# Performance work log

Hardware: AMD Instinct MI355X
Metric: run time of the kernel (lower is better)

The kernel has to match this reference:

```python
import jax, jax.numpy as jnp
import numpy as np


def _conv(x, w, b, stride, pad):
    y = jax.lax.conv_general_dilated(x, w, (stride, stride), [(pad, pad), (pad, pad)],
                                     dimension_numbers=('NCHW', 'OIHW', 'NCHW'))
    return y + b[None, :, None, None]


def _deconv(x, w, b, stride):
    # kernel == stride, VALID padding -> exact x`stride` upsample
    y = jax.lax.conv_transpose(x, w, (stride, stride), 'VALID',
                               dimension_numbers=('NCHW', 'OIHW', 'NCHW'))
    return y + b[None, :, None, None]


def _fuse(feat):
    # TransformerFusion: per-pixel scaled dot-product attention over cav axis, keep ego (cav 0)
    n, C, H, W = feat.shape
    t = feat.reshape(n, C, H * W).transpose(2, 0, 1)            # (HW, n, C)
    scores = jnp.einsum('pnc,pmc->pnm', t, t) / np.float32(np.sqrt(C))
    attn = jax.nn.softmax(scores, axis=-1)
    out = jnp.einsum('pnm,pmc->pnc', attn, t)                   # (HW, n, C)
    return out[:, 0, :].T.reshape(C, H, W)


def _sta(x, w1, w2):
    # CBAM-style channel attention: shared MLP on avg-pool and max-pool
    avg = x.mean(axis=(2, 3))                                   # (B, C)
    mx = x.max(axis=(2, 3))
    fc = lambda z: jax.nn.relu(z @ w1.T) @ w2.T
    return jax.nn.sigmoid(fc(avg) + fc(mx))[:, :, None, None]


def _forward(x, historical_x, time_delay, record_len,
             enh_w, enh_b, b0_w, b0_b, b1_w, b1_b, b2_w, b2_b,
             d0_w, d0_b, d1_w, d1_b, d2_w, d2_b, sta_w1, sta_w2):
    aoi = time_delay[0]                                         # (N + 2,)
    enw = jnp.tanh(enh_w * (1.0 / (aoi + 0.1)) + enh_b) + 1.0   # EnhanceWeight, batched
    # loop mapping: t=0 -> x[0]; t=1,2 -> historical[0,1]; t=3,4 -> x[1,2]
    x = x * jnp.stack([enw[0], enw[3], enw[4]])[:, None, None, None]
    historical_x = historical_x * enw[1:3][:, None, None, None]
    historical_x = jax.nn.relu(_conv(historical_x, b0_w, b0_b, 2, 1))  # backbone.blocks[0]

    ups = []
    x = jax.nn.relu(_conv(x, b0_w, b0_b, 2, 1))                 # level 0: (N,64,128,256)
    ups.append(_conv(_fuse(x[:record_len])[None], d0_w, d0_b, 1, 0))
    x = jax.nn.relu(_conv(x, b1_w, b1_b, 2, 1))                 # level 1: (N,128,64,128)
    ups.append(_deconv(_fuse(x[:record_len])[None], d1_w, d1_b, 2))
    x = jax.nn.relu(_conv(x, b2_w, b2_b, 2, 1))                 # level 2: (N,256,32,64)
    ups.append(_deconv(_fuse(x[:record_len])[None], d2_w, d2_b, 4))
    ups.append(historical_x[0:1])
    ups.append(historical_x[1:2])
    x_fuse = jnp.concatenate(ups, axis=1)                       # (1, 512, 128, 256)
    return _sta(x_fuse, sta_w1, sta_w2) * x_fuse


def setup_inputs() -> dict:
    key = jax.random.key(0)
    ks = jax.random.split(key, 16)
    w = lambda k, shape, fan_in: (jax.random.normal(k, shape, jnp.float32)
                                  * np.float32(np.sqrt(2.0 / fan_in)))
    N, C, H, W = 3, 64, 256, 512
    return {
        'x': jax.random.normal(ks[0], (N, C, H, W), jnp.float32),
        'historical_x': jax.random.normal(ks[1], (2, C, H, W), jnp.float32),
        'psm_single': jax.random.normal(ks[2], (N, 2, H // 2, W // 2), jnp.float32),
        'pairwise_t_matrix': jax.random.normal(ks[3], (1, N + 2, N + 2, 4, 4), jnp.float32),
        'time_delay': jax.random.uniform(ks[4], (1, N + 2), jnp.float32),
        'record_len': 3,
        'enh_w': jax.random.normal(ks[5], (), jnp.float32),
        'enh_b': jnp.zeros((), jnp.float32),
        'b0_w': w(ks[6], (64, 64, 3, 3), 64 * 9),  'b0_b': jnp.zeros((64,), jnp.float32),
        'b1_w': w(ks[7], (128, 64, 3, 3), 64 * 9), 'b1_b': jnp.zeros((128,), jnp.float32),
        'b2_w': w(ks[8], (256, 128, 3, 3), 128 * 9), 'b2_b': jnp.zeros((256,), jnp.float32),
        'd0_w': w(ks[9], (128, 64, 1, 1), 64),     'd0_b': jnp.zeros((128,), jnp.float32),
        'd1_w': w(ks[10], (128, 128, 2, 2), 128 * 4), 'd1_b': jnp.zeros((128,), jnp.float32),
        'd2_w': w(ks[11], (128, 256, 4, 4), 256 * 16), 'd2_b': jnp.zeros((128,), jnp.float32),
        'sta_w1': w(ks[12], (32, 512), 512),
        'sta_w2': w(ks[13], (512, 32), 32),
    }


def reference(x, historical_x, psm_single, pairwise_t_matrix, time_delay, record_len,
              enh_w, enh_b, b0_w, b0_b, b1_w, b1_b, b2_w, b2_b,
              d0_w, d0_b, d1_w, d1_b, d2_w, d2_b, sta_w1, sta_w2):
    # psm_single / pairwise_t_matrix are accepted but unused by HPHA's math path
    return _forward(x, historical_x, time_delay, record_len,
                    enh_w, enh_b, b0_w, b0_b, b1_w, b1_b, b2_w, b2_b,
                    d0_w, d0_b, d1_w, d1_b, d2_w, d2_b, sta_w1, sta_w2)
```

## Files before the change

### kernel.cpp

```cpp
#include <hip/hip_runtime.h>
#include <math.h>

#define HW0 32768

typedef __attribute__((ext_vector_type(8))) short short8v;
typedef __attribute__((ext_vector_type(4))) float f32x4;

static const size_t WS_SCALES = 0;
static const size_t WS_MEAN   = 64;
static const size_t WS_MAX    = 64 + 512;
static const size_t WS_GATE   = 64 + 1024;
static const size_t WS_L0X    = 2048;
static const size_t WS_L1     = WS_L0X + (size_t)3*64*128*256;
static const size_t WS_L2     = WS_L1  + (size_t)3*128*64*128;
static const size_t WS_F0     = WS_L2  + (size_t)3*256*32*64;
static const size_t WS_F1     = WS_F0  + (size_t)64*128*256;
static const size_t WS_F2     = WS_F1  + (size_t)128*64*128;
static const size_t WS_W0P    = WS_F2  + (size_t)256*32*64;
static const size_t WS_W1P    = WS_W0P + 18432;
static const size_t WS_W2P    = WS_W1P + 36864;
static const size_t WS_U0P    = WS_W2P + 147456;
static const size_t WS_U1P    = WS_U0P + 4096;
static const size_t WS_U2P    = WS_U1P + 32768;
static const size_t WS_STG    = WS_U2P + 262144;

__device__ inline unsigned short f2bf(float x) {
  unsigned u = __float_as_uint(x);
  unsigned r = ((u >> 16) & 1u) + 0x7FFFu;
  return (unsigned short)((u + r) >> 16);
}

__global__ void prep_k(const float* __restrict__ td, const float* __restrict__ ew,
                       const float* __restrict__ eb, float* __restrict__ scales) {
  int i = threadIdx.x;
  if (i < 5) {
    float e = tanhf(ew[0] * (1.0f / (td[i] + 0.1f)) + eb[0]) + 1.0f;
    const int slot[5] = {0, 3, 4, 1, 2};
    scales[slot[i]] = e;
  }
}

__global__ __launch_bounds__(256) void repack_k(const float* __restrict__ in,
                                                unsigned short* __restrict__ outh,
                                                int C, int H, int W) {
  __shared__ unsigned short lds[64 * 72];
  const int t = threadIdx.x;
  const int cbn = C >> 6;
  const int n  = blockIdx.z / cbn;
  const int cb = (blockIdx.z % cbn) << 6;
  const int h  = blockIdx.y;
  const int w0 = blockIdx.x << 6;
  const int wl = t & 63, cg = t >> 6;
  const float* ip = in + (((size_t)n * C + cb) * H + h) * W + w0;
#pragma unroll 4
  for (int cj = 0; cj < 16; ++cj) {
    int c = cg * 16 + cj;
    lds[wl * 72 + c] = f2bf(ip[(size_t)c * H * W + wl]);
  }
  __syncthreads();
  const int pw = t >> 2, ch = t & 3;
  unsigned short* op = outh + ((size_t)n * H * W + (size_t)h * W + w0 + pw) * C + cb;
#pragma unroll
  for (int it = 0; it < 2; ++it) {
    int c0 = (ch + it * 4) * 8;
    *(uint4*)(op + c0) = *(const uint4*)(lds + pw * 72 + c0);
  }
}

__global__ void pack_w_k(const float* __restrict__ W, unsigned short* __restrict__ wp,
                         int Cout, int Cin, int NK) {
  int t = blockIdx.x * 256 + threadIdx.x;
  if (t >= Cout * NK * 4) return;
  int co = t / (NK * 4); int rem = t - co * (NK * 4); int s = rem >> 2; int js = rem & 3;
  int cog = co >> 4; int l = js * 16 + (co & 15);
  unsigned short v[8];
#pragma unroll
  for (int j = 0; j < 8; ++j) {
    int k = s * 32 + js * 8 + j;
    int tap = k / Cin, ci = k - tap * Cin;
    int ky = tap / 3, kx = tap - ky * 3;
    v[j] = f2bf(W[(((size_t)co * Cin + ci) * 3 + ky) * 3 + kx]);
  }
  *(uint4*)(wp + ((size_t)(cog * NK + s) * 64 + l) * 8) = *(uint4*)v;
}

__global__ void pack_dw_k(const float* __restrict__ W, unsigned short* __restrict__ wp,
                          int M, int K, int NK, int mode) {
  int t = blockIdx.x * 256 + threadIdx.x;
  if (t >= M * NK * 4) return;
  int m = t / (NK * 4); int rem = t - m * (NK * 4); int s = rem >> 2; int js = rem & 3;
  int mt = m >> 4; int l = js * 16 + (m & 15);
  unsigned short v[8];
#pragma unroll
  for (int j = 0; j < 8; ++j) {
    int k = s * 32 + js * 8 + j;
    size_t idx;
    if (mode == 0) {
      idx = (size_t)m * K + k;
    } else if (mode == 1) {
      int o = m >> 2, r = (m >> 1) & 1, c = m & 1;
      idx = ((size_t)o * K + k) * 4 + (1 - r) * 2 + (1 - c);
    } else {
      int o = m >> 4, r = (m >> 2) & 3, c = m & 3;
      idx = ((size_t)o * K + k) * 16 + (3 - r) * 4 + (3 - c);
    }
    v[j] = f2bf(W[idx]);
  }
  *(uint4*)(wp + ((size_t)(mt * NK + s) * 64 + l) * 8) = *(uint4*)v;
}

template <int CIN, int COG>
__global__ __launch_bounds__(256) void conv_mfma_k(
    const unsigned short* __restrict__ inh, const unsigned short* __restrict__ wp,
    const float* __restrict__ bias, float* __restrict__ out,
    const float* __restrict__ scales, int Cout, int Hout, int Wout, int cogrp) {
  constexpr int NK = (9 * CIN) / 32;
  extern __shared__ unsigned short wlds[];
  const int tid = threadIdx.x, lane = tid & 63, wv = tid >> 6;
  const int Hin = Hout * 2, Win = Wout * 2;
  const int n   = blockIdx.z / cogrp;
  const int cg  = blockIdx.z % cogrp;
  const int co0 = cg * (COG * 16);
  const int h   = blockIdx.y;
  const int w0  = blockIdx.x * 64;

  {
    const float4* src = (const float4*)(wp + (size_t)(co0 >> 4) * NK * 64 * 8);
    float4* dst = (float4*)wlds;
    for (int i = tid; i < COG * NK * 64; i += 256) dst[i] = src[i];
  }
  __syncthreads();

  const int px = w0 + wv * 16 + (lane & 15);
  const int js = lane >> 4;
  const unsigned short* inp = inh + (size_t)n * CIN * Hin * Win;

  f32x4 acc[COG];
#pragma unroll
  for (int c = 0; c < COG; ++c) acc[c] = (f32x4){0.f, 0.f, 0.f, 0.f};

  const short8v bz = {0, 0, 0, 0, 0, 0, 0, 0};
  for (int s = 0; s < NK; ++s) {
    const int tap = (s * 32) / CIN;
    const int ci  = (s * 32) % CIN + js * 8;
    const int ky = tap / 3, kx = tap - ky * 3;
    const int iy = 2 * h + ky - 1;
    short8v b = bz;
    if (iy >= 0) {
      const int ix = 2 * px + kx - 1;
      const unsigned short* p = inp + ((size_t)iy * Win + (ix < 0 ? 0 : ix)) * CIN + ci;
      short8v v = *(const short8v*)p;
      if (ix >= 0) b = v;
    }
#pragma unroll
    for (int c = 0; c < COG; ++c) {
      short8v a = *(const short8v*)&wlds[((c * NK + s) * 64 + lane) * 8];
      acc[c] = __builtin_amdgcn_mfma_f32_16x16x32_bf16(a, b, acc[c], 0, 0, 0);
    }
  }

  const float sc = scales ? scales[n] : 1.0f;
#pragma unroll
  for (int c = 0; c < COG; ++c) {
#pragma unroll
    for (int r = 0; r < 4; ++r) {
      const int co = co0 + c * 16 + js * 4 + r;
      float v = fmaxf(acc[c][r] * sc + bias[co], 0.f);
      out[(((size_t)n * Cout + co) * Hout + h) * Wout + px] = v;
    }
  }
}

template <int C>
__global__ __launch_bounds__(256) void fuse2_k(const float* __restrict__ in,
                                               unsigned short* __restrict__ outh,
                                               int HW, float inv_sqrtC) {
  constexpr int LPP = C / 16;
  constexpr int PPW = 64 / LPP;
  const int tid = threadIdx.x;
  const int lane = tid & 63, wv = tid >> 6;
  const int g = lane / PPW;
  const int p = blockIdx.x * (4 * PPW) + wv * PPW + (lane % PPW);
  const float* b0 = in + (size_t)(g * 16) * HW + p;
  const float* b1 = b0 + (size_t)C * HW;
  const float* b2 = b1 + (size_t)C * HW;
  float va[16], vb[16], vd[16];
  float d00 = 0.f, d01 = 0.f, d02 = 0.f;
#pragma unroll
  for (int j = 0; j < 16; ++j) {
    va[j] = b0[(size_t)j * HW];
    vb[j] = b1[(size_t)j * HW];
    vd[j] = b2[(size_t)j * HW];
    d00 += va[j] * va[j]; d01 += va[j] * vb[j]; d02 += va[j] * vd[j];
  }
#pragma unroll
  for (int off = PPW; off < 64; off <<= 1) {
    d00 += __shfl_xor(d00, off);
    d01 += __shfl_xor(d01, off);
    d02 += __shfl_xor(d02, off);
  }
  float s0 = d00 * inv_sqrtC, s1 = d01 * inv_sqrtC, s2 = d02 * inv_sqrtC;
  float m = fmaxf(s0, fmaxf(s1, s2));
  float e0 = expf(s0 - m), e1 = expf(s1 - m), e2 = expf(s2 - m);
  float inv = 1.0f / (e0 + e1 + e2);
  float a0 = e0 * inv, a1 = e1 * inv, a2 = e2 * inv;
  unsigned short tmp[16];
#pragma unroll
  for (int j = 0; j < 16; ++j)
    tmp[j] = f2bf(a0 * va[j] + a1 * vb[j] + a2 * vd[j]);
  unsigned short* o0 = outh + (size_t)p * C + g * 16;
  *(uint4*)(o0)     = *(const uint4*)(tmp);
  *(uint4*)(o0 + 8) = *(const uint4*)(tmp + 8);
}

template <int K, int MT, int EPI>
__global__ __launch_bounds__(256) void up_mfma_k(
    const unsigned short* __restrict__ fh, const unsigned short* __restrict__ wp,
    const float* __restrict__ bias, float* __restrict__ out) {
  constexpr int NK = K / 32;
  extern __shared__ unsigned short wlds[];
  const int tid = threadIdx.x, lane = tid & 63, wv = tid >> 6;
  const int mt0 = blockIdx.y * MT;
  {
    const float4* src = (const float4*)(wp + (size_t)mt0 * NK * 64 * 8);
    float4* dst = (float4*)wlds;
    for (int i = tid; i < MT * NK * 64; i += 256) dst[i] = src[i];
  }
  __syncthreads();

  const int px = blockIdx.x * 64 + wv * 16 + (lane & 15);
  const int js = lane >> 4;
  const unsigned short* bp = fh + (size_t)px * K + js * 8;

  f32x4 acc[MT];
#pragma unroll
  for (int t = 0; t < MT; ++t) acc[t] = (f32x4){0.f, 0.f, 0.f, 0.f};

#pragma unroll
  for (int s = 0; s < NK; ++s) {
    short8v b = *(const short8v*)(bp + s * 32);
#pragma unroll
    for (int t = 0; t < MT; ++t) {
      short8v a = *(const short8v*)&wlds[((t * NK + s) * 64 + lane) * 8];
      acc[t] = __builtin_amdgcn_mfma_f32_16x16x32_bf16(a, b, acc[t], 0, 0, 0);
    }
  }

  if constexpr (EPI == 0) {
#pragma unroll
    for (int t = 0; t < MT; ++t) {
      const int o = (mt0 + t) * 16 + js * 4;
#pragma unroll
      for (int r = 0; r < 4; ++r)
        out[(size_t)(o + r) * HW0 + px] = acc[t][r] + bias[o + r];
    }
  } else if constexpr (EPI == 1) {
    const int h = px >> 7, w = px & 127;
#pragma unroll
    for (int t = 0; t < MT; ++t) {
      const int o = (mt0 + t) * 4 + js;
      const float b = bias[o];
      float* base = out + (size_t)o * HW0 + (size_t)(2 * h) * 256 + 2 * w;
      *(float2*)base         = make_float2(acc[t][0] + b, acc[t][1] + b);
      *(float2*)(base + 256) = make_float2(acc[t][2] + b, acc[t][3] + b);
    }
  } else {
    const int h = px >> 6, w = px & 63;
#pragma unroll
    for (int t = 0; t < MT; ++t) {
      const int o = mt0 + t;
      const float b = bias[o];
      float4 v = make_float4(acc[t][0] + b, acc[t][1] + b, acc[t][2] + b, acc[t][3] + b);
      *(float4*)(out + (size_t)o * HW0 + (size_t)(4 * h + js) * 256 + 4 * w) = v;
    }
  }
}

__global__ __launch_bounds__(256) void sta_reduce_k(const float* __restrict__ xf,
                                                    float* __restrict__ mean,
                                                    float* __restrict__ mx) {
  const int c = blockIdx.x;
  const float* p = xf + (size_t)c * HW0;
  float s = 0.f, m = -1e30f;
  for (int i = threadIdx.x * 4; i < HW0; i += 1024) {
    float4 v = *(const float4*)(p + i);
    s += v.x + v.y + v.z + v.w;
    m = fmaxf(m, fmaxf(fmaxf(v.x, v.y), fmaxf(v.z, v.w)));
  }
#pragma unroll
  for (int off = 32; off; off >>= 1) {
    s += __shfl_down(s, off);
    m = fmaxf(m, __shfl_down(m, off));
  }
  __shared__ float ss[4], sm[4];
  if ((threadIdx.x & 63) == 0) { ss[threadIdx.x >> 6] = s; sm[threadIdx.x >> 6] = m; }
  __syncthreads();
  if (threadIdx.x == 0) {
    float S = ss[0] + ss[1] + ss[2] + ss[3];
    float M = fmaxf(fmaxf(sm[0], sm[1]), fmaxf(sm[2], sm[3]));
    mean[c] = S * (1.0f / 32768.0f);
    mx[c] = M;
  }
}

__global__ void sta_gate_k(const float* __restrict__ mean, const float* __restrict__ mx,
                           const float* __restrict__ w1, const float* __restrict__ w2,
                           float* __restrict__ gate) {
  __shared__ float havg[32], hmax[32];
  const int t = threadIdx.x;
  if (t < 32) {
    float sa = 0.f, sm = 0.f;
    for (int cc = 0; cc < 512; ++cc) {
      float w = w1[t * 512 + cc];
      sa += mean[cc] * w;
      sm += mx[cc] * w;
    }
    havg[t] = fmaxf(sa, 0.f);
    hmax[t] = fmaxf(sm, 0.f);
  }
  __syncthreads();
  float g = 0.f;
  for (int j = 0; j < 32; ++j) g += (havg[j] + hmax[j]) * w2[t * 32 + j];
  gate[t] = 1.0f / (1.0f + expf(-g));
}

__global__ __launch_bounds__(256) void sta_scale_k(float* __restrict__ xf,
                                                   const float* __restrict__ gate) {
  const size_t i = (size_t)(blockIdx.x * 256 + threadIdx.x) * 4;
  float4 v = *(const float4*)(xf + i);
  const float g = gate[i >> 15];
  v.x *= g; v.y *= g; v.z *= g; v.w *= g;
  *(float4*)(xf + i) = v;
}

extern "C" void kernel_launch(void* const* d_in, const int* in_sizes, int n_in,
                              void* d_out, int out_size, void* d_ws, size_t ws_size,
                              hipStream_t stream) {
  const float* x    = (const float*)d_in[0];
  const float* hist = (const float*)d_in[1];
  const float* td   = (const float*)d_in[4];
  const float* ew   = (const float*)d_in[6];
  const float* eb   = (const float*)d_in[7];
  const float* b0w  = (const float*)d_in[8];
  const float* b0b  = (const float*)d_in[9];
  const float* b1w  = (const float*)d_in[10];
  const float* b1b  = (const float*)d_in[11];
  const float* b2w  = (const float*)d_in[12];
  const float* b2b  = (const float*)d_in[13];
  const float* d0w  = (const float*)d_in[14];
  const float* d0b  = (const float*)d_in[15];
  const float* d1w  = (const float*)d_in[16];
  const float* d1b  = (const float*)d_in[17];
  const float* d2w  = (const float*)d_in[18];
  const float* d2b  = (const float*)d_in[19];
  const float* w1   = (const float*)d_in[20];
  const float* w2   = (const float*)d_in[21];

  float* out = (float*)d_out;
  float* ws  = (float*)d_ws;

  float* scales = ws + WS_SCALES;
  float* l0x = ws + WS_L0X;
  float* l1  = ws + WS_L1;
  float* l2  = ws + WS_L2;
  unsigned short* f0h = (unsigned short*)(ws + WS_F0);
  unsigned short* f1h = (unsigned short*)(ws + WS_F1);
  unsigned short* f2h = (unsigned short*)(ws + WS_F2);
  unsigned short* w0p = (unsigned short*)(ws + WS_W0P);
  unsigned short* w1p = (unsigned short*)(ws + WS_W1P);
  unsigned short* w2p = (unsigned short*)(ws + WS_W2P);
  unsigned short* u0p = (unsigned short*)(ws + WS_U0P);
  unsigned short* u1p = (unsigned short*)(ws + WS_U1P);
  unsigned short* u2p = (unsigned short*)(ws + WS_U2P);
  unsigned short* stg = (unsigned short*)(ws + WS_STG);

  prep_k<<<1, 64, 0, stream>>>(td, ew, eb, scales);
  pack_w_k<<<18, 256, 0, stream>>>(b0w, w0p, 64, 64, 18);
  pack_w_k<<<36, 256, 0, stream>>>(b1w, w1p, 128, 64, 18);
  pack_w_k<<<144, 256, 0, stream>>>(b2w, w2p, 256, 128, 36);
  pack_dw_k<<<4, 256, 0, stream>>>(d0w, u0p, 128, 64, 2, 0);
  pack_dw_k<<<32, 256, 0, stream>>>(d1w, u1p, 512, 128, 4, 1);
  pack_dw_k<<<256, 256, 0, stream>>>(d2w, u2p, 2048, 256, 8, 2);

  repack_k<<<dim3(8, 256, 3), 256, 0, stream>>>(x, stg, 64, 256, 512);
  conv_mfma_k<64, 4><<<dim3(4, 128, 3), 256, 73728, stream>>>(
      stg, w0p, b0b, l0x, scales, 64, 128, 256, 1);

  repack_k<<<dim3(8, 256, 2), 256, 0, stream>>>(hist, stg, 64, 256, 512);
  conv_mfma_k<64, 4><<<dim3(4, 128, 2), 256, 73728, stream>>>(
      stg, w0p, b0b, out + (size_t)384 * HW0, scales + 3, 64, 128, 256, 1);

  fuse2_k<64><<<512, 256, 0, stream>>>(l0x, f0h, 32768, 0.125f);
  up_mfma_k<64, 8, 0><<<dim3(512, 1), 256, 16384, stream>>>(f0h, u0p, d0b, out);

  repack_k<<<dim3(4, 128, 3), 256, 0, stream>>>(l0x, stg, 64, 128, 256);
  conv_mfma_k<64, 4><<<dim3(2, 64, 6), 256, 73728, stream>>>(
      stg, w1p, b1b, l1, nullptr, 128, 64, 128, 2);
  fuse2_k<128><<<256, 256, 0, stream>>>(l1, f1h, 8192, 0.0883883476f);
  up_mfma_k<128, 8, 1><<<dim3(128, 4), 256, 32768, stream>>>(
      f1h, u1p, d1b, out + (size_t)128 * HW0);

  repack_k<<<dim3(2, 64, 6), 256, 0, stream>>>(l1, stg, 128, 64, 128);
  conv_mfma_k<128, 2><<<dim3(1, 32, 24), 256, 73728, stream>>>(
      stg, w2p, b2b, l2, nullptr, 256, 32, 64, 8);
  fuse2_k<256><<<128, 256, 0, stream>>>(l2, f2h, 2048, 0.0625f);
  up_mfma_k<256, 4, 2><<<dim3(32, 32), 256, 32768, stream>>>(
      f2h, u2p, d2b, out + (size_t)256 * HW0);

  sta_reduce_k<<<512, 256, 0, stream>>>(out, ws + WS_MEAN, ws + WS_MAX);
  sta_gate_k<<<1, 512, 0, stream>>>(ws + WS_MEAN, ws + WS_MAX, w1, w2, ws + WS_GATE);
  sta_scale_k<<<16384, 256, 0, stream>>>(out, ws + WS_GATE);
}
```

Before: 505.1 us.

## Fuse repacks into conv epilogue, merge fuse+up0, batch weight packing

The conv epilogue now also writes a bf16 NHWC copy of its output, so the separate repack kernels before level-1 and level-2 convs are removed. The level-0 attention fusion and 1x1 upsample are merged into one kernel that keeps the fused tile in swizzled LDS instead of round-tripping through global memory. All weight-packing and scale-prep launches are collapsed into a single kernel. In exchange the conv epilogue does extra bf16 stores and the workspace grows.

```diff
diff --git a/kernel.cpp b/kernel.cpp
--- a/kernel.cpp
+++ b/kernel.cpp
@@ -8,21 +8,22 @@
 
 static const size_t WS_SCALES = 0;
 static const size_t WS_MEAN   = 64;
-static const size_t WS_MAX    = 64 + 512;
-static const size_t WS_GATE   = 64 + 1024;
+static const size_t WS_MAX    = 576;
+static const size_t WS_GATE   = 1088;
 static const size_t WS_L0X    = 2048;
 static const size_t WS_L1     = WS_L0X + (size_t)3*64*128*256;
 static const size_t WS_L2     = WS_L1  + (size_t)3*128*64*128;
-static const size_t WS_F0     = WS_L2  + (size_t)3*256*32*64;
-static const size_t WS_F1     = WS_F0  + (size_t)64*128*256;
-static const size_t WS_F2     = WS_F1  + (size_t)128*64*128;
-static const size_t WS_W0P    = WS_F2  + (size_t)256*32*64;
+static const size_t WS_F1     = WS_L2  + (size_t)3*256*32*64;
+static const size_t WS_F2     = WS_F1  + 524288;
+static const size_t WS_W0P    = WS_F2  + 262144;
 static const size_t WS_W1P    = WS_W0P + 18432;
 static const size_t WS_W2P    = WS_W1P + 36864;
 static const size_t WS_U0P    = WS_W2P + 147456;
 static const size_t WS_U1P    = WS_U0P + 4096;
 static const size_t WS_U2P    = WS_U1P + 32768;
-static const size_t WS_STG    = WS_U2P + 262144;
+static const size_t WS_L0H    = WS_U2P + 262144;
+static const size_t WS_L1H    = WS_L0H + 3145728;
+static const size_t WS_STG    = WS_L1H + 1572864;
 
 __device__ inline unsigned short f2bf(float x) {
   unsigned u = __float_as_uint(x);
@@ -30,13 +31,76 @@
   return (unsigned short)((u + r) >> 16);
 }
 
-__global__ void prep_k(const float* __restrict__ td, const float* __restrict__ ew,
-                       const float* __restrict__ eb, float* __restrict__ scales) {
-  int i = threadIdx.x;
-  if (i < 5) {
-    float e = tanhf(ew[0] * (1.0f / (td[i] + 0.1f)) + eb[0]) + 1.0f;
-    const int slot[5] = {0, 3, 4, 1, 2};
-    scales[slot[i]] = e;
+__device__ inline void pack_w_body(int t, const float* __restrict__ W,
+                                   unsigned short* __restrict__ wp,
+                                   int Cout, int Cin, int NK) {
+  if (t >= Cout * NK * 4) return;
+  int co = t / (NK * 4); int rem = t - co * (NK * 4); int s = rem >> 2; int js = rem & 3;
+  int cog = co >> 4; int l = js * 16 + (co & 15);
+  unsigned short v[8];
+#pragma unroll
+  for (int j = 0; j < 8; ++j) {
+    int k = s * 32 + js * 8 + j;
+    int tap = k / Cin, ci = k - tap * Cin;
+    int ky = tap / 3, kx = tap - ky * 3;
+    v[j] = f2bf(W[(((size_t)co * Cin + ci) * 3 + ky) * 3 + kx]);
+  }
+  *(uint4*)(wp + ((size_t)(cog * NK + s) * 64 + l) * 8) = *(uint4*)v;
+}
+
+__device__ inline void pack_dw_body(int t, const float* __restrict__ W,
+                                    unsigned short* __restrict__ wp,
+                                    int M, int K, int NK, int mode) {
+  if (t >= M * NK * 4) return;
+  int m = t / (NK * 4); int rem = t - m * (NK * 4); int s = rem >> 2; int js = rem & 3;
+  int mt = m >> 4; int l = js * 16 + (m & 15);
+  unsigned short v[8];
+#pragma unroll
+  for (int j = 0; j < 8; ++j) {
+    int k = s * 32 + js * 8 + j;
+    size_t idx;
+    if (mode == 0) {
+      idx = (size_t)m * K + k;
+    } else if (mode == 1) {
+      int o = m >> 2, r = (m >> 1) & 1, c = m & 1;
+      idx = ((size_t)o * K + k) * 4 + (1 - r) * 2 + (1 - c);
+    } else {
+      int o = m >> 4, r = (m >> 2) & 3, c = m & 3;
+      idx = ((size_t)o * K + k) * 16 + (3 - r) * 4 + (3 - c);
+    }
+    v[j] = f2bf(W[idx]);
+  }
+  *(uint4*)(wp + ((size_t)(mt * NK + s) * 64 + l) * 8) = *(uint4*)v;
+}
+
+__global__ __launch_bounds__(256) void pack_all_k(
+    const float* __restrict__ td, const float* __restrict__ ew,
+    const float* __restrict__ eb, float* __restrict__ scales,
+    const float* __restrict__ b0w, unsigned short* __restrict__ w0p,
+    const float* __restrict__ b1w, unsigned short* __restrict__ w1p,
+    const float* __restrict__ b2w, unsigned short* __restrict__ w2p,
+    const float* __restrict__ d0w, unsigned short* __restrict__ u0p,
+    const float* __restrict__ d1w, unsigned short* __restrict__ u1p,
+    const float* __restrict__ d2w, unsigned short* __restrict__ u2p) {
+  const int b = blockIdx.x, tid = threadIdx.x;
+  if (b == 0) {
+    if (tid < 5) {
+      float e = tanhf(ew[0] * (1.0f / (td[tid] + 0.1f)) + eb[0]) + 1.0f;
+      const int slot[5] = {0, 3, 4, 1, 2};
+      scales[slot[tid]] = e;
+    }
+  } else if (b < 19) {
+    pack_w_body((b - 1) * 256 + tid, b0w, w0p, 64, 64, 18);
+  } else if (b < 55) {
+    pack_w_body((b - 19) * 256 + tid, b1w, w1p, 128, 64, 18);
+  } else if (b < 199) {
+    pack_w_body((b - 55) * 256 + tid, b2w, w2p, 256, 128, 36);
+  } else if (b < 203) {
+    pack_dw_body((b - 199) * 256 + tid, d0w, u0p, 128, 64, 2, 0);
+  } else if (b < 235) {
+    pack_dw_body((b - 203) * 256 + tid, d1w, u1p, 512, 128, 4, 1);
+  } else {
+    pack_dw_body((b - 235) * 256 + tid, d2w, u2p, 2048, 256, 8, 2);
   }
 }
 
@@ -67,52 +131,11 @@
   }
 }
 
-__global__ void pack_w_k(const float* __restrict__ W, unsigned short* __restrict__ wp,
-                         int Cout, int Cin, int NK) {
-  int t = blockIdx.x * 256 + threadIdx.x;
-  if (t >= Cout * NK * 4) return;
-  int co = t / (NK * 4); int rem = t - co * (NK * 4); int s = rem >> 2; int js = rem & 3;
-  int cog = co >> 4; int l = js * 16 + (co & 15);
-  unsigned short v[8];
-#pragma unroll
-  for (int j = 0; j < 8; ++j) {
-    int k = s * 32 + js * 8 + j;
-    int tap = k / Cin, ci = k - tap * Cin;
-    int ky = tap / 3, kx = tap - ky * 3;
-    v[j] = f2bf(W[(((size_t)co * Cin + ci) * 3 + ky) * 3 + kx]);
-  }
-  *(uint4*)(wp + ((size_t)(cog * NK + s) * 64 + l) * 8) = *(uint4*)v;
-}
-
-__global__ void pack_dw_k(const float* __restrict__ W, unsigned short* __restrict__ wp,
-                          int M, int K, int NK, int mode) {
-  int t = blockIdx.x * 256 + threadIdx.x;
-  if (t >= M * NK * 4) return;
-  int m = t / (NK * 4); int rem = t - m * (NK * 4); int s = rem >> 2; int js = rem & 3;
-  int mt = m >> 4; int l = js * 16 + (m & 15);
-  unsigned short v[8];
-#pragma unroll
-  for (int j = 0; j < 8; ++j) {
-    int k = s * 32 + js * 8 + j;
-    size_t idx;
-    if (mode == 0) {
-      idx = (size_t)m * K + k;
-    } else if (mode == 1) {
-      int o = m >> 2, r = (m >> 1) & 1, c = m & 1;
-      idx = ((size_t)o * K + k) * 4 + (1 - r) * 2 + (1 - c);
-    } else {
-      int o = m >> 4, r = (m >> 2) & 3, c = m & 3;
-      idx = ((size_t)o * K + k) * 16 + (3 - r) * 4 + (3 - c);
-    }
-    v[j] = f2bf(W[idx]);
-  }
-  *(uint4*)(wp + ((size_t)(mt * NK + s) * 64 + l) * 8) = *(uint4*)v;
-}
-
 template <int CIN, int COG>
 __global__ __launch_bounds__(256) void conv_mfma_k(
     const unsigned short* __restrict__ inh, const unsigned short* __restrict__ wp,
     const float* __restrict__ bias, float* __restrict__ out,
+    unsigned short* __restrict__ outh,
     const float* __restrict__ scales, int Cout, int Hout, int Wout, int cogrp) {
   constexpr int NK = (9 * CIN) / 32;
   extern __shared__ unsigned short wlds[];
@@ -160,13 +183,21 @@
   }
 
   const float sc = scales ? scales[n] : 1.0f;
+  unsigned short* oph = outh
+      ? outh + ((size_t)n * Hout * Wout + (size_t)h * Wout + px) * Cout + co0
+      : nullptr;
 #pragma unroll
   for (int c = 0; c < COG; ++c) {
+    float vv[4];
 #pragma unroll
     for (int r = 0; r < 4; ++r) {
       const int co = co0 + c * 16 + js * 4 + r;
-      float v = fmaxf(acc[c][r] * sc + bias[co], 0.f);
-      out[(((size_t)n * Cout + co) * Hout + h) * Wout + px] = v;
+      vv[r] = fmaxf(acc[c][r] * sc + bias[co], 0.f);
+      out[(((size_t)n * Cout + co) * Hout + h) * Wout + px] = vv[r];
+    }
+    if (oph) {
+      unsigned short hv[4] = {f2bf(vv[0]), f2bf(vv[1]), f2bf(vv[2]), f2bf(vv[3])};
+      *(uint2*)(oph + c * 16 + js * 4) = *(const uint2*)hv;
     }
   }
 }
@@ -213,17 +244,88 @@
   *(uint4*)(o0 + 8) = *(const uint4*)(tmp + 8);
 }
 
+__global__ __launch_bounds__(256) void fuse_up0_k(const float* __restrict__ in,
+                                                  const unsigned short* __restrict__ wp,
+                                                  const float* __restrict__ bias,
+                                                  float* __restrict__ out) {
+  __shared__ unsigned short wlds[8192];
+  __shared__ unsigned short pbuf[4096];
+  const int tid = threadIdx.x, lane = tid & 63, wv = tid >> 6;
+  {
+    const uint4* src = (const uint4*)wp;
+    uint4* dst = (uint4*)wlds;
+    for (int i = tid; i < 1024; i += 256) dst[i] = src[i];
+  }
+  const int g = lane >> 4;
+  const int pl = wv * 16 + (lane & 15);
+  const int p = blockIdx.x * 64 + pl;
+  const float* b0 = in + (size_t)(g * 16) * HW0 + p;
+  const float* b1 = b0 + (size_t)64 * HW0;
+  const float* b2 = b1 + (size_t)64 * HW0;
+  float va[16], vb[16], vd[16];
+  float d00 = 0.f, d01 = 0.f, d02 = 0.f;
+#pragma unroll
+  for (int j = 0; j < 16; ++j) {
+    va[j] = b0[(size_t)j * HW0];
+    vb[j] = b1[(size_t)j * HW0];
+    vd[j] = b2[(size_t)j * HW0];
+    d00 += va[j] * va[j]; d01 += va[j] * vb[j]; d02 += va[j] * vd[j];
+  }
+#pragma unroll
+  for (int off = 16; off < 64; off <<= 1) {
+    d00 += __shfl_xor(d00, off);
+    d01 += __shfl_xor(d01, off);
+    d02 += __shfl_xor(d02, off);
+  }
+  float s0 = d00 * 0.125f, s1 = d01 * 0.125f, s2 = d02 * 0.125f;
+  float m = fmaxf(s0, fmaxf(s1, s2));
+  float e0 = expf(s0 - m), e1 = expf(s1 - m), e2 = expf(s2 - m);
+  float inv = 1.0f / (e0 + e1 + e2);
+  float a0 = e0 * inv, a1 = e1 * inv, a2 = e2 * inv;
+  unsigned short tmp[16];
+#pragma unroll
+  for (int j = 0; j < 16; ++j)
+    tmp[j] = f2bf(a0 * va[j] + a1 * vb[j] + a2 * vd[j]);
+  const unsigned swz = (unsigned)((pl & 7) << 4);
+  const unsigned base = (unsigned)(pl * 128 + g * 32);
+  *(uint4*)((char*)pbuf + (base ^ swz))        = *(const uint4*)tmp;
+  *(uint4*)((char*)pbuf + ((base + 16) ^ swz)) = *(const uint4*)(tmp + 8);
+  __syncthreads();
+
+  const int js = lane >> 4;
+  f32x4 acc[8];
+#pragma unroll
+  for (int t = 0; t < 8; ++t) acc[t] = (f32x4){0.f, 0.f, 0.f, 0.f};
+#pragma unroll
+  for (int s = 0; s < 2; ++s) {
+    const unsigned rb = (unsigned)(pl * 128 + (s * 32 + js * 8) * 2) ^ swz;
+    short8v b = *(const short8v*)((const char*)pbuf + rb);
+#pragma unroll
+    for (int t = 0; t < 8; ++t) {
+      short8v a = *(const short8v*)&wlds[((t * 2 + s) * 64 + lane) * 8];
+      acc[t] = __builtin_amdgcn_mfma_f32_16x16x32_bf16(a, b, acc[t], 0, 0, 0);
+    }
+  }
+#pragma unroll
+  for (int t = 0; t < 8; ++t) {
+    const int o = t * 16 + js * 4;
+#pragma unroll
+    for (int r = 0; r < 4; ++r)
+      out[(size_t)(o + r) * HW0 + p] = acc[t][r] + bias[o + r];
+  }
+}
+
 template <int K, int MT, int EPI>
 __global__ __launch_bounds__(256) void up_mfma_k(
     const unsigned short* __restrict__ fh, const unsigned short* __restrict__ wp,
     const float* __restrict__ bias, float* __restrict__ out) {
   constexpr int NK = K / 32;
-  extern __shared__ unsigned short wlds[];
+  extern __shared__ unsigned short uplds[];
   const int tid = threadIdx.x, lane = tid & 63, wv = tid >> 6;
   const int mt0 = blockIdx.y * MT;
   {
     const float4* src = (const float4*)(wp + (size_t)mt0 * NK * 64 * 8);
-    float4* dst = (float4*)wlds;
+    float4* dst = (float4*)uplds;
     for (int i = tid; i < MT * NK * 64; i += 256) dst[i] = src[i];
   }
   __syncthreads();
@@ -241,20 +343,12 @@
     short8v b = *(const short8v*)(bp + s * 32);
 #pragma unroll
     for (int t = 0; t < MT; ++t) {
-      short8v a = *(const short8v*)&wlds[((t * NK + s) * 64 + lane) * 8];
+      short8v a = *(const short8v*)&uplds[((t * NK + s) * 64 + lane) * 8];
       acc[t] = __builtin_amdgcn_mfma_f32_16x16x32_bf16(a, b, acc[t], 0, 0, 0);
     }
   }
 
-  if constexpr (EPI == 0) {
-#pragma unroll
-    for (int t = 0; t < MT; ++t) {
-      const int o = (mt0 + t) * 16 + js * 4;
-#pragma unroll
-      for (int r = 0; r < 4; ++r)
-        out[(size_t)(o + r) * HW0 + px] = acc[t][r] + bias[o + r];
-    }
-  } else if constexpr (EPI == 1) {
+  if constexpr (EPI == 1) {
     const int h = px >> 7, w = px & 127;
 #pragma unroll
     for (int t = 0; t < MT; ++t) {
@@ -363,7 +457,6 @@
   float* l0x = ws + WS_L0X;
   float* l1  = ws + WS_L1;
   float* l2  = ws + WS_L2;
-  unsigned short* f0h = (unsigned short*)(ws + WS_F0);
   unsigned short* f1h = (unsigned short*)(ws + WS_F1);
   unsigned short* f2h = (unsigned short*)(ws + WS_F2);
   unsigned short* w0p = (unsigned short*)(ws + WS_W0P);
@@ -372,37 +465,32 @@
   unsigned short* u0p = (unsigned short*)(ws + WS_U0P);
   unsigned short* u1p = (unsigned short*)(ws + WS_U1P);
   unsigned short* u2p = (unsigned short*)(ws + WS_U2P);
+  unsigned short* l0h = (unsigned short*)(ws + WS_L0H);
+  unsigned short* l1h = (unsigned short*)(ws + WS_L1H);
   unsigned short* stg = (unsigned short*)(ws + WS_STG);
 
-  prep_k<<<1, 64, 0, stream>>>(td, ew, eb, scales);
-  pack_w_k<<<18, 256, 0, stream>>>(b0w, w0p, 64, 64, 18);
-  pack_w_k<<<36, 256, 0, stream>>>(b1w, w1p, 128, 64, 18);
-  pack_w_k<<<144, 256, 0, stream>>>(b2w, w2p, 256, 128, 36);
-  pack_dw_k<<<4, 256, 0, stream>>>(d0w, u0p, 128, 64, 2, 0);
-  pack_dw_k<<<32, 256, 0, stream>>>(d1w, u1p, 512, 128, 4, 1);
-  pack_dw_k<<<256, 256, 0, stream>>>(d2w, u2p, 2048, 256, 8, 2);
+  pack_all_k<<<491, 256, 0, stream>>>(td, ew, eb, scales,
+                                      b0w, w0p, b1w, w1p, b2w, w2p,
+                                      d0w, u0p, d1w, u1p, d2w, u2p);
 
   repack_k<<<dim3(8, 256, 3), 256, 0, stream>>>(x, stg, 64, 256, 512);
   conv_mfma_k<64, 4><<<dim3(4, 128, 3), 256, 73728, stream>>>(
-      stg, w0p, b0b, l0x, scales, 64, 128, 256, 1);
+      stg, w0p, b0b, l0x, l0h, scales, 64, 128, 256, 1);
 
   repack_k<<<dim3(8, 256, 2), 256, 0, stream>>>(hist, stg, 64, 256, 512);
   conv_mfma_k<64, 4><<<dim3(4, 128, 2), 256, 73728, stream>>>(
-      stg, w0p, b0b, out + (size_t)384 * HW0, scales + 3, 64, 128, 256, 1);
-
-  fuse2_k<64><<<512, 256, 0, stream>>>(l0x, f0h, 32768, 0.125f);
-  up_mfma_k<64, 8, 0><<<dim3(512, 1), 256, 16384, stream>>>(f0h, u0p, d0b, out);
-
-  repack_k<<<dim3(4, 128, 3), 256, 0, stream>>>(l0x, stg, 64, 128, 256);
+      stg, w0p, b0b, out + (size_t)384 * HW0, nullptr, scales + 3, 64, 128, 256, 1);
+
+  fuse_up0_k<<<512, 256, 0, stream>>>(l0x, u0p, d0b, out);
+
   conv_mfma_k<64, 4><<<dim3(2, 64, 6), 256, 73728, stream>>>(
-      stg, w1p, b1b, l1, nullptr, 128, 64, 128, 2);
+      l0h, w1p, b1b, l1, l1h, nullptr, 128, 64, 128, 2);
   fuse2_k<128><<<256, 256, 0, stream>>>(l1, f1h, 8192, 0.0883883476f);
   up_mfma_k<128, 8, 1><<<dim3(128, 4), 256, 32768, stream>>>(
       f1h, u1p, d1b, out + (size_t)128 * HW0);
 
-  repack_k<<<dim3(2, 64, 6), 256, 0, stream>>>(l1, stg, 128, 64, 128);
   conv_mfma_k<128, 2><<<dim3(1, 32, 24), 256, 73728, stream>>>(
-      stg, w2p, b2b, l2, nullptr, 256, 32, 64, 8);
+      l1h, w2p, b2b, l2, nullptr, nullptr, 256, 32, 64, 8);
   fuse2_k<256><<<128, 256, 0, stream>>>(l2, f2h, 2048, 0.0625f);
   up_mfma_k<256, 4, 2><<<dim3(32, 32), 256, 32768, stream>>>(
       f2h, u2p, d2b, out + (size_t)256 * HW0);
```

New measurement: 477.6 us. -5.4%, faster.
